# Performance work log

Measured on AMD Instinct MI355X. Metric: run time of the kernel, lower is better.

Reference implementation:

```python
import jax, jax.numpy as jnp
import numpy as np

TEMPERATURE = 0.1
NORM_EPS = 1e-12   # F.normalize default eps
LOSS_EPS = 1e-6

def _l2norm_c(x):
    # L2-normalize along channel dim (axis=1), matching F.normalize(dim=1)
    n = jnp.sqrt(jnp.sum(x * x, axis=1, keepdims=True))
    return x / jnp.maximum(n, NORM_EPS)

def setup_inputs() -> dict:
    key = jax.random.key(0)
    k1, k2, k3 = jax.random.split(key, 3)
    N, C, H, W = 8, 64, 64, 64
    rgb_map = jax.random.normal(k1, (N, C, H, W), dtype=jnp.float32)
    ir_map = jax.random.normal(k2, (N, C, H, W), dtype=jnp.float32)
    targets = jax.random.randint(k3, (N,), 0, 2)  # unused by the forward math
    return {"rgb_map": rgb_map, "ir_map": ir_map, "targets": targets}

def reference(rgb_map, ir_map, targets):
    N, C, H, W = rgb_map.shape
    rgb = _l2norm_c(rgb_map).reshape(N, C, H * W)   # [N, C, P]
    ir = _l2norm_c(ir_map).reshape(N, C, H * W)     # [N, C, P]
    # [N, P, P] similarity, then temperature exp
    logit = jnp.exp(jnp.einsum('ncp,ncq->npq', rgb, ir) / TEMPERATURE)
    pos = jnp.trace(logit, axis1=1, axis2=2)        # diagonal (positive) sum per sample
    tot = jnp.sum(logit, axis=(-1, -2))             # full row/col sum per sample
    loss = -jnp.log(pos / (tot + LOSS_EPS)).mean()
    return loss
```

## Files before the change

kernel.cpp:

```cpp
#include <hip/hip_runtime.h>

#define N_ 8
#define C_ 64
#define P_ 4096

typedef float f32x4 __attribute__((ext_vector_type(4)));
typedef float f32x2 __attribute__((ext_vector_type(2)));
typedef short bf16x8 __attribute__((ext_vector_type(8)));

__device__ __forceinline__ unsigned short f2bf(float f) {
  unsigned int u = __builtin_bit_cast(unsigned int, f);
  u = (u + 0x7fffu + ((u >> 16) & 1u)) >> 16;
  return (unsigned short)u;
}

__device__ __forceinline__ float exp2appr(float x) {
  const int i = (int)__builtin_fmaf(x, 8388608.0f, 1064992209.0f);
  return __builtin_bit_cast(float, i);
}

__global__ void __launch_bounds__(256) norm_transpose(
    const float* __restrict__ rgb, const float* __restrict__ ir,
    unsigned short* __restrict__ rgbnT, unsigned short* __restrict__ irnT) {
  const int tid = threadIdx.x;
  const int half = tid >> 7;
  const int pl = tid & 127;
  const int gp = blockIdx.x * 128 + pl;
  const int n = gp >> 12;
  const int p = gp & (P_ - 1);
  const float* src = (blockIdx.y == 0) ? rgb : ir;
  unsigned short* dst = (blockIdx.y == 0) ? rgbnT : irnT;
  const float SC = 14.4269504088896340736f;
  const float* col = src + (size_t)n * C_ * P_ + (size_t)(half * 32) * P_ + p;
  float v[32];
  float ss = 0.f;
#pragma unroll
  for (int c = 0; c < 32; ++c) {
    v[c] = col[(size_t)c * P_];
    ss += v[c] * v[c];
  }
  __shared__ float ssq[2][128];
  ssq[half][pl] = ss;
  __syncthreads();
  const float tot = ssq[0][pl] + ssq[1][pl];
  float inv = 1.0f / fmaxf(sqrtf(tot), 1e-12f);
  if (blockIdx.y == 0) inv *= SC;
  const int gx = (blockIdx.y == 0) ? 0 : (p & 7);
  unsigned short* o = dst + (size_t)gp * C_;
#pragma unroll
  for (int gi = 0; gi < 4; ++gi) {
    bf16x8 pack;
#pragma unroll
    for (int j = 0; j < 8; ++j) pack[j] = (short)f2bf(v[gi * 8 + j] * inv);
    const int gg = half * 4 + gi;
    *reinterpret_cast<bf16x8*>(o + (gg ^ gx) * 8) = pack;
  }
}

__device__ __forceinline__ void stage_tile(const unsigned short* src,
                                           unsigned short* dst, int tid,
                                           int wid) {
#pragma unroll
  for (int r = 0; r < 2; ++r) {
    __builtin_amdgcn_global_load_lds(
        (const __attribute__((address_space(1))) void*)(src +
                                                        (size_t)(r * 256 + tid) * 8),
        (__attribute__((address_space(3))) void*)(dst + (r * 256 + wid * 64) * 8),
        16, 0, 0);
  }
}

__global__ void __launch_bounds__(256) gemm_exp_reduce(
    const unsigned short* __restrict__ aT, const unsigned short* __restrict__ bT,
    float* __restrict__ partials) {
  const int lin = blockIdx.x;
  const int n = lin & 7;
  const int local = lin >> 3;
  const int pc = local & 15;
  const int qc = local >> 4;
  const int tid = threadIdx.x;
  const int lane = tid & 63;
  const int wid = tid >> 6;
  const int pbase = pc * 256 + wid * 64;
  const int q0 = qc * 512;
  const unsigned short* A = aT + (size_t)n * P_ * C_;
  const unsigned short* B = bT + (size_t)n * P_ * C_;
  const int r16 = lane & 15;
  const int kofs = (lane >> 4) * 8;

  __shared__ __align__(16) unsigned short bs0[64 * 64];
  __shared__ __align__(16) unsigned short bs1[64 * 64];
  __shared__ __align__(16) unsigned short bs2[64 * 64];
  __shared__ __align__(16) unsigned short bs3[64 * 64];

  bf16x8 af[2][4];
#pragma unroll
  for (int ks = 0; ks < 2; ++ks)
#pragma unroll
    for (int mi = 0; mi < 4; ++mi)
      af[ks][mi] = *reinterpret_cast<const bf16x8*>(
          A + (size_t)(pbase + mi * 16 + r16) * C_ + ks * 32 + kofs);

  stage_tile(B + (size_t)(q0 + 0 * 64) * C_, bs0, tid, wid);
  stage_tile(B + (size_t)(q0 + 1 * 64) * C_, bs1, tid, wid);
  stage_tile(B + (size_t)(q0 + 2 * 64) * C_, bs2, tid, wid);

  unsigned short *pcur = bs0, *pnx1 = bs1, *pnx2 = bs2, *pnx3 = bs3;

  const f32x4 zc = (f32x4)(0.f);
  f32x2 ch2[8];
#pragma unroll
  for (int k = 0; k < 8; ++k) ch2[k] = (f32x2)(0.f);
  float pos = 0.f;
  const int col = lane & 15;
  const int rowb = (lane >> 4) * 4;

#pragma unroll 1
  for (int t = 0; t < 8; ++t) {
    asm volatile("s_waitcnt vmcnt(4)" ::: "memory");
    __builtin_amdgcn_sched_barrier(0);
    __builtin_amdgcn_s_barrier();

    int s = t + 3;
    if (s >= 8) s -= 8;
    stage_tile(B + (size_t)(q0 + s * 64) * C_, pnx3, tid, wid);

    const unsigned short* bp = pcur;
    bf16x8 bf_[2][4];
#pragma unroll
    for (int ks = 0; ks < 2; ++ks)
#pragma unroll
      for (int ni = 0; ni < 4; ++ni) {
        const int row = ni * 16 + r16;
        const int seg = ks * 4 + (lane >> 4);
        bf_[ks][ni] = *reinterpret_cast<const bf16x8*>(
            bp + row * 64 + ((seg ^ (lane & 7)) * 8));
      }

    f32x4 acc[4][4];
    __builtin_amdgcn_s_setprio(1);
#pragma unroll
    for (int mi = 0; mi < 4; ++mi)
#pragma unroll
      for (int ni = 0; ni < 4; ++ni)
        acc[mi][ni] = __builtin_amdgcn_mfma_f32_16x16x32_bf16(
            af[0][mi], bf_[0][ni], zc, 0, 0, 0);
#pragma unroll
    for (int mi = 0; mi < 4; ++mi)
#pragma unroll
      for (int ni = 0; ni < 4; ++ni)
        acc[mi][ni] = __builtin_amdgcn_mfma_f32_16x16x32_bf16(
            af[1][mi], bf_[1][ni], acc[mi][ni], 0, 0, 0);
    __builtin_amdgcn_s_setprio(0);

#pragma unroll
    for (int mi = 0; mi < 4; ++mi)
#pragma unroll
      for (int ni = 0; ni < 4; ++ni) {
        const int base = ((mi * 4 + ni) & 3) * 2;
        const f32x4 v = acc[mi][ni];
        f32x2 a0, a1;
        a0[0] = v[0]; a0[1] = v[1];
        a1[0] = v[2]; a1[1] = v[3];
        const f32x2 f0 = a0 * 8388608.0f + (f32x2)(1064992209.0f);
        const f32x2 f1 = a1 * 8388608.0f + (f32x2)(1064992209.0f);
        f32x2 e0, e1;
        e0[0] = __builtin_bit_cast(float, (int)f0[0]);
        e0[1] = __builtin_bit_cast(float, (int)f0[1]);
        e1[0] = __builtin_bit_cast(float, (int)f1[0]);
        e1[1] = __builtin_bit_cast(float, (int)f1[1]);
        ch2[base] += e0;
        ch2[base + 1] += e1;
      }
    const int qb = q0 + t * 64;
    if (pbase == qb) {
#pragma unroll
      for (int mi = 0; mi < 4; ++mi)
#pragma unroll
        for (int r = 0; r < 4; ++r)
          if (rowb + r == col) pos += exp2appr(acc[mi][mi][r]);
    }

    unsigned short* tmp = pcur;
    pcur = pnx1;
    pnx1 = pnx2;
    pnx2 = pnx3;
    pnx3 = tmp;
  }

  f32x2 sum2 = ((ch2[0] + ch2[1]) + (ch2[2] + ch2[3])) +
               ((ch2[4] + ch2[5]) + (ch2[6] + ch2[7]));
  float tot = sum2[0] + sum2[1];
#pragma unroll
  for (int off = 32; off > 0; off >>= 1) {
    tot += __shfl_down(tot, off);
    pos += __shfl_down(pos, off);
  }
  __shared__ float sb[8];
  if (lane == 0) { sb[wid * 2] = pos; sb[wid * 2 + 1] = tot; }
  __syncthreads();
  if (tid == 0) {
    const float pp = sb[0] + sb[2] + sb[4] + sb[6];
    const float tt = sb[1] + sb[3] + sb[5] + sb[7];
    const int bid = n * 128 + pc * 8 + qc;
    partials[bid * 2] = pp;
    partials[bid * 2 + 1] = tt;
  }
}

__global__ void __launch_bounds__(1024) finalize(
    const float* __restrict__ partials, float* __restrict__ out) {
  const int tid = threadIdx.x;
  const int lane = tid & 63, wid = tid >> 6;
  __shared__ float sp[16], st[16], sl[8];
  const int n = tid >> 7;
  const int i = tid & 127;
  float p = partials[(n * 128 + i) * 2];
  float t = partials[(n * 128 + i) * 2 + 1];
#pragma unroll
  for (int off = 32; off > 0; off >>= 1) {
    p += __shfl_down(p, off);
    t += __shfl_down(t, off);
  }
  if (lane == 0) { sp[wid] = p; st[wid] = t; }
  __syncthreads();
  if (tid < 8) {
    const float pp = sp[2 * tid] + sp[2 * tid + 1];
    const float tt = st[2 * tid] + st[2 * tid + 1];
    sl[tid] = -logf(pp / (tt + 1e-6f));
  }
  __syncthreads();
  if (tid == 0) {
    float loss = 0.f;
#pragma unroll
    for (int k = 0; k < 8; ++k) loss += sl[k];
    out[0] = loss * (1.0f / N_);
  }
}

extern "C" void kernel_launch(void* const* d_in, const int* in_sizes, int n_in,
                              void* d_out, int out_size, void* d_ws, size_t ws_size,
                              hipStream_t stream) {
  const float* rgb = (const float*)d_in[0];
  const float* ir = (const float*)d_in[1];
  float* out = (float*)d_out;

  unsigned short* rgbnT = (unsigned short*)d_ws;
  unsigned short* irnT = rgbnT + (size_t)N_ * P_ * C_;
  float* partials = (float*)(irnT + (size_t)N_ * P_ * C_);

  dim3 g1(N_ * P_ / 128, 2);
  norm_transpose<<<g1, 256, 0, stream>>>(rgb, ir, rgbnT, irnT);

  gemm_exp_reduce<<<1024, 256, 0, stream>>>(rgbnT, irnT, partials);

  finalize<<<1, 1024, 0, stream>>>(partials, out);
}
```

Baseline: 39.28 us.

## Load B tiles straight into registers with double buffering instead of LDS staging

The GEMM kernel no longer stages B tiles into a four-deep LDS ring through global_load_lds, and drops the per-iteration block barrier. Each wave now issues its own inline-asm global_load_dwordx4 loads of its swizzled B fragments into two register buffers, prefetching the tile after next while computing the current one. The aim is to remove LDS round trips and block synchronization from the inner loop. In exchange, every wave re-reads the same B data from cache, register pressure rises, and the last iterations prefetch past the tile range instead of wrapping, which reads data that is never used.

Measured after the change: 45.42 us. +15.6%, slower.

```diff
diff --git a/kernel.cpp b/kernel.cpp
--- a/kernel.cpp
+++ b/kernel.cpp
@@ -7,6 +7,7 @@
 typedef float f32x4 __attribute__((ext_vector_type(4)));
 typedef float f32x2 __attribute__((ext_vector_type(2)));
 typedef short bf16x8 __attribute__((ext_vector_type(8)));
+typedef unsigned long long u64;
 
 __device__ __forceinline__ unsigned short f2bf(float f) {
   unsigned int u = __builtin_bit_cast(unsigned int, f);
@@ -54,19 +55,6 @@
     for (int j = 0; j < 8; ++j) pack[j] = (short)f2bf(v[gi * 8 + j] * inv);
     const int gg = half * 4 + gi;
     *reinterpret_cast<bf16x8*>(o + (gg ^ gx) * 8) = pack;
-  }
-}
-
-__device__ __forceinline__ void stage_tile(const unsigned short* src,
-                                           unsigned short* dst, int tid,
-                                           int wid) {
-#pragma unroll
-  for (int r = 0; r < 2; ++r) {
-    __builtin_amdgcn_global_load_lds(
-        (const __attribute__((address_space(1))) void*)(src +
-                                                        (size_t)(r * 256 + tid) * 8),
-        (__attribute__((address_space(3))) void*)(dst + (r * 256 + wid * 64) * 8),
-        16, 0, 0);
   }
 }
 
@@ -88,24 +76,39 @@
   const int r16 = lane & 15;
   const int kofs = (lane >> 4) * 8;
 
-  __shared__ __align__(16) unsigned short bs0[64 * 64];
-  __shared__ __align__(16) unsigned short bs1[64 * 64];
-  __shared__ __align__(16) unsigned short bs2[64 * 64];
-  __shared__ __align__(16) unsigned short bs3[64 * 64];
-
-  bf16x8 af[2][4];
+  u64 ba[8];
 #pragma unroll
   for (int ks = 0; ks < 2; ++ks)
 #pragma unroll
-    for (int mi = 0; mi < 4; ++mi)
-      af[ks][mi] = *reinterpret_cast<const bf16x8*>(
-          A + (size_t)(pbase + mi * 16 + r16) * C_ + ks * 32 + kofs);
-
-  stage_tile(B + (size_t)(q0 + 0 * 64) * C_, bs0, tid, wid);
-  stage_tile(B + (size_t)(q0 + 1 * 64) * C_, bs1, tid, wid);
-  stage_tile(B + (size_t)(q0 + 2 * 64) * C_, bs2, tid, wid);
-
-  unsigned short *pcur = bs0, *pnx1 = bs1, *pnx2 = bs2, *pnx3 = bs3;
+    for (int ni = 0; ni < 4; ++ni) {
+      const int row = ni * 16 + r16;
+      const int seg = ks * 4 + (lane >> 4);
+      const int fo = row * 128 + ((seg ^ (lane & 7)) * 16);
+      ba[ks * 4 + ni] = (u64)(size_t)B + (u64)(q0 * 128 + fo);
+    }
+
+  f32x4 af[2][4];
+#pragma unroll
+  for (int ks = 0; ks < 2; ++ks)
+#pragma unroll
+    for (int mi = 0; mi < 4; ++mi) {
+      const u64 aa = (u64)(size_t)(A + (size_t)(pbase + mi * 16 + r16) * C_ +
+                                   ks * 32 + kofs);
+      asm volatile("global_load_dwordx4 %0, %1, off"
+                   : "=v"(af[ks][mi]) : "v"(aa));
+    }
+
+  f32x4 br0[2][4], br1[2][4];
+#pragma unroll
+  for (int j = 0; j < 8; ++j)
+    asm volatile("global_load_dwordx4 %0, %1, off"
+                 : "=v"(br0[j >> 2][j & 3]) : "v"(ba[j]));
+#pragma unroll
+  for (int j = 0; j < 8; ++j)
+    asm volatile("global_load_dwordx4 %0, %1, off"
+                 : "=v"(br1[j >> 2][j & 3]) : "v"(ba[j] + 8192));
+#pragma unroll
+  for (int j = 0; j < 8; ++j) ba[j] += 16384;
 
   const f32x4 zc = (f32x4)(0.f);
   f32x2 ch2[8];
@@ -115,27 +118,12 @@
   const int col = lane & 15;
   const int rowb = (lane >> 4) * 4;
 
-#pragma unroll 1
+#pragma unroll 2
   for (int t = 0; t < 8; ++t) {
-    asm volatile("s_waitcnt vmcnt(4)" ::: "memory");
+    asm volatile("s_waitcnt vmcnt(8)" ::: "memory");
     __builtin_amdgcn_sched_barrier(0);
-    __builtin_amdgcn_s_barrier();
-
-    int s = t + 3;
-    if (s >= 8) s -= 8;
-    stage_tile(B + (size_t)(q0 + s * 64) * C_, pnx3, tid, wid);
-
-    const unsigned short* bp = pcur;
-    bf16x8 bf_[2][4];
-#pragma unroll
-    for (int ks = 0; ks < 2; ++ks)
-#pragma unroll
-      for (int ni = 0; ni < 4; ++ni) {
-        const int row = ni * 16 + r16;
-        const int seg = ks * 4 + (lane >> 4);
-        bf_[ks][ni] = *reinterpret_cast<const bf16x8*>(
-            bp + row * 64 + ((seg ^ (lane & 7)) * 8));
-      }
+
+    f32x4(&br)[2][4] = (t & 1) ? br1 : br0;
 
     f32x4 acc[4][4];
     __builtin_amdgcn_s_setprio(1);
@@ -144,13 +132,15 @@
 #pragma unroll
       for (int ni = 0; ni < 4; ++ni)
         acc[mi][ni] = __builtin_amdgcn_mfma_f32_16x16x32_bf16(
-            af[0][mi], bf_[0][ni], zc, 0, 0, 0);
+            __builtin_bit_cast(bf16x8, af[0][mi]),
+            __builtin_bit_cast(bf16x8, br[0][ni]), zc, 0, 0, 0);
 #pragma unroll
     for (int mi = 0; mi < 4; ++mi)
 #pragma unroll
       for (int ni = 0; ni < 4; ++ni)
         acc[mi][ni] = __builtin_amdgcn_mfma_f32_16x16x32_bf16(
-            af[1][mi], bf_[1][ni], acc[mi][ni], 0, 0, 0);
+            __builtin_bit_cast(bf16x8, af[1][mi]),
+            __builtin_bit_cast(bf16x8, br[1][ni]), acc[mi][ni], 0, 0, 0);
     __builtin_amdgcn_s_setprio(0);
 
 #pragma unroll
@@ -181,11 +171,13 @@
           if (rowb + r == col) pos += exp2appr(acc[mi][mi][r]);
     }
 
-    unsigned short* tmp = pcur;
-    pcur = pnx1;
-    pnx1 = pnx2;
-    pnx2 = pnx3;
-    pnx3 = tmp;
+    __builtin_amdgcn_sched_barrier(0);
+#pragma unroll
+    for (int j = 0; j < 8; ++j)
+      asm volatile("global_load_dwordx4 %0, %1, off"
+                   : "=v"(br[j >> 2][j & 3]) : "v"(ba[j]));
+#pragma unroll
+    for (int j = 0; j < 8; ++j) ba[j] += 8192;
   }
 
   f32x2 sum2 = ((ch2[0] + ch2[1]) + (ch2[2] + ch2[3])) +
```

## Fuse normalization, GEMM-exp reduction and finalize into one kernel

Applied to the files above, without the earlier changes.

Merges the three kernels into one. Each block now computes L2 norms and builds bf16 operands straight from the raw fp32 inputs: the whole 512-column B slab goes into LDS up front, and the A fragments are loaded into registers. The last block to finish, found with an atomic counter, does the final loss reduction. This removes two launches and the round-trip of the transposed bf16 intermediates through global memory. In exchange, fp32 inputs are re-read redundantly across blocks (A about 8x, B about 16x) using strided column loads. The large 64KB LDS footprint may cut occupancy, and a memset launch is added.

New measurement: 55.40 us. +41.0%, slower.

```diff
diff --git a/kernel.cpp b/kernel.cpp
--- a/kernel.cpp
+++ b/kernel.cpp
@@ -19,60 +19,10 @@
   return __builtin_bit_cast(float, i);
 }
 
-__global__ void __launch_bounds__(256) norm_transpose(
+__global__ void __launch_bounds__(256) pixcon_fused(
     const float* __restrict__ rgb, const float* __restrict__ ir,
-    unsigned short* __restrict__ rgbnT, unsigned short* __restrict__ irnT) {
-  const int tid = threadIdx.x;
-  const int half = tid >> 7;
-  const int pl = tid & 127;
-  const int gp = blockIdx.x * 128 + pl;
-  const int n = gp >> 12;
-  const int p = gp & (P_ - 1);
-  const float* src = (blockIdx.y == 0) ? rgb : ir;
-  unsigned short* dst = (blockIdx.y == 0) ? rgbnT : irnT;
-  const float SC = 14.4269504088896340736f;
-  const float* col = src + (size_t)n * C_ * P_ + (size_t)(half * 32) * P_ + p;
-  float v[32];
-  float ss = 0.f;
-#pragma unroll
-  for (int c = 0; c < 32; ++c) {
-    v[c] = col[(size_t)c * P_];
-    ss += v[c] * v[c];
-  }
-  __shared__ float ssq[2][128];
-  ssq[half][pl] = ss;
-  __syncthreads();
-  const float tot = ssq[0][pl] + ssq[1][pl];
-  float inv = 1.0f / fmaxf(sqrtf(tot), 1e-12f);
-  if (blockIdx.y == 0) inv *= SC;
-  const int gx = (blockIdx.y == 0) ? 0 : (p & 7);
-  unsigned short* o = dst + (size_t)gp * C_;
-#pragma unroll
-  for (int gi = 0; gi < 4; ++gi) {
-    bf16x8 pack;
-#pragma unroll
-    for (int j = 0; j < 8; ++j) pack[j] = (short)f2bf(v[gi * 8 + j] * inv);
-    const int gg = half * 4 + gi;
-    *reinterpret_cast<bf16x8*>(o + (gg ^ gx) * 8) = pack;
-  }
-}
-
-__device__ __forceinline__ void stage_tile(const unsigned short* src,
-                                           unsigned short* dst, int tid,
-                                           int wid) {
-#pragma unroll
-  for (int r = 0; r < 2; ++r) {
-    __builtin_amdgcn_global_load_lds(
-        (const __attribute__((address_space(1))) void*)(src +
-                                                        (size_t)(r * 256 + tid) * 8),
-        (__attribute__((address_space(3))) void*)(dst + (r * 256 + wid * 64) * 8),
-        16, 0, 0);
-  }
-}
-
-__global__ void __launch_bounds__(256) gemm_exp_reduce(
-    const unsigned short* __restrict__ aT, const unsigned short* __restrict__ bT,
-    float* __restrict__ partials) {
+    float* __restrict__ par, unsigned* __restrict__ cnt,
+    float* __restrict__ out) {
   const int lin = blockIdx.x;
   const int n = lin & 7;
   const int local = lin >> 3;
@@ -81,31 +31,83 @@
   const int tid = threadIdx.x;
   const int lane = tid & 63;
   const int wid = tid >> 6;
-  const int pbase = pc * 256 + wid * 64;
+  const int p0 = pc * 256;
   const int q0 = qc * 512;
-  const unsigned short* A = aT + (size_t)n * P_ * C_;
-  const unsigned short* B = bT + (size_t)n * P_ * C_;
+  const int pbase = p0 + wid * 64;
+  const float* Araw = rgb + (size_t)n * C_ * P_;
+  const float* Braw = ir + (size_t)n * C_ * P_;
+
+  __shared__ __align__(16) unsigned short bsm[512 * 64];
+  __shared__ float ssqA[256];
+  __shared__ float sb[8];
+  __shared__ float fp[8], ft[8];
+  __shared__ unsigned rank_s;
+
+  {
+    float ss = 0.f;
+    const float* colp = Araw + p0 + tid;
+#pragma unroll 8
+    for (int c = 0; c < 64; ++c) {
+      const float x = colp[(size_t)c * P_];
+      ss = __builtin_fmaf(x, x, ss);
+    }
+    ssqA[tid] = ss;
+  }
+
+  {
+    const float* colq = Braw + q0 + 2 * tid;
+    float ss0 = 0.f, ss1 = 0.f;
+#pragma unroll 8
+    for (int c = 0; c < 64; ++c) {
+      const f32x2 v = *reinterpret_cast<const f32x2*>(colq + (size_t)c * P_);
+      ss0 = __builtin_fmaf(v[0], v[0], ss0);
+      ss1 = __builtin_fmaf(v[1], v[1], ss1);
+    }
+    const float inv0 = 1.0f / fmaxf(sqrtf(ss0), 1e-12f);
+    const float inv1 = 1.0f / fmaxf(sqrtf(ss1), 1e-12f);
+    const int r0 = 2 * tid, r1 = 2 * tid + 1;
+    unsigned short* w0 = bsm + r0 * 64;
+    unsigned short* w1 = bsm + r1 * 64;
+#pragma unroll 1
+    for (int g = 0; g < 8; ++g) {
+      bf16x8 pk0, pk1;
+#pragma unroll
+      for (int j = 0; j < 8; ++j) {
+        const f32x2 v =
+            *reinterpret_cast<const f32x2*>(colq + (size_t)(g * 8 + j) * P_);
+        pk0[j] = (short)f2bf(v[0] * inv0);
+        pk1[j] = (short)f2bf(v[1] * inv1);
+      }
+      *reinterpret_cast<bf16x8*>(w0 + ((g ^ (r0 & 7)) * 8)) = pk0;
+      *reinterpret_cast<bf16x8*>(w1 + ((g ^ (r1 & 7)) * 8)) = pk1;
+    }
+  }
+
+  __syncthreads();
+
   const int r16 = lane & 15;
   const int kofs = (lane >> 4) * 8;
-
-  __shared__ __align__(16) unsigned short bs0[64 * 64];
-  __shared__ __align__(16) unsigned short bs1[64 * 64];
-  __shared__ __align__(16) unsigned short bs2[64 * 64];
-  __shared__ __align__(16) unsigned short bs3[64 * 64];
-
+  const float SC = 14.4269504088896340736f;
+  float invA[4];
+#pragma unroll
+  for (int mi = 0; mi < 4; ++mi) {
+    const int rrel = wid * 64 + mi * 16 + r16;
+    invA[mi] = SC / fmaxf(sqrtf(ssqA[rrel]), 1e-12f);
+  }
   bf16x8 af[2][4];
 #pragma unroll
   for (int ks = 0; ks < 2; ++ks)
 #pragma unroll
-    for (int mi = 0; mi < 4; ++mi)
-      af[ks][mi] = *reinterpret_cast<const bf16x8*>(
-          A + (size_t)(pbase + mi * 16 + r16) * C_ + ks * 32 + kofs);
-
-  stage_tile(B + (size_t)(q0 + 0 * 64) * C_, bs0, tid, wid);
-  stage_tile(B + (size_t)(q0 + 1 * 64) * C_, bs1, tid, wid);
-  stage_tile(B + (size_t)(q0 + 2 * 64) * C_, bs2, tid, wid);
-
-  unsigned short *pcur = bs0, *pnx1 = bs1, *pnx2 = bs2, *pnx3 = bs3;
+    for (int mi = 0; mi < 4; ++mi) {
+      const float* src = Araw + pbase + mi * 16 + r16;
+      bf16x8 pk;
+#pragma unroll
+      for (int j = 0; j < 8; ++j) {
+        const float x = src[(size_t)(ks * 32 + kofs + j) * P_];
+        pk[j] = (short)f2bf(x * invA[mi]);
+      }
+      af[ks][mi] = pk;
+    }
 
   const f32x4 zc = (f32x4)(0.f);
   f32x2 ch2[8];
@@ -117,15 +119,7 @@
 
 #pragma unroll 1
   for (int t = 0; t < 8; ++t) {
-    asm volatile("s_waitcnt vmcnt(4)" ::: "memory");
-    __builtin_amdgcn_sched_barrier(0);
-    __builtin_amdgcn_s_barrier();
-
-    int s = t + 3;
-    if (s >= 8) s -= 8;
-    stage_tile(B + (size_t)(q0 + s * 64) * C_, pnx3, tid, wid);
-
-    const unsigned short* bp = pcur;
+    const unsigned short* bp = bsm + t * 64 * 64;
     bf16x8 bf_[2][4];
 #pragma unroll
     for (int ks = 0; ks < 2; ++ks)
@@ -180,12 +174,6 @@
         for (int r = 0; r < 4; ++r)
           if (rowb + r == col) pos += exp2appr(acc[mi][mi][r]);
     }
-
-    unsigned short* tmp = pcur;
-    pcur = pnx1;
-    pnx1 = pnx2;
-    pnx2 = pnx3;
-    pnx3 = tmp;
   }
 
   f32x2 sum2 = ((ch2[0] + ch2[1]) + (ch2[2] + ch2[3])) +
@@ -196,45 +184,41 @@
     tot += __shfl_down(tot, off);
     pos += __shfl_down(pos, off);
   }
-  __shared__ float sb[8];
   if (lane == 0) { sb[wid * 2] = pos; sb[wid * 2 + 1] = tot; }
   __syncthreads();
+
   if (tid == 0) {
     const float pp = sb[0] + sb[2] + sb[4] + sb[6];
     const float tt = sb[1] + sb[3] + sb[5] + sb[7];
-    const int bid = n * 128 + pc * 8 + qc;
-    partials[bid * 2] = pp;
-    partials[bid * 2 + 1] = tt;
-  }
-}
-
-__global__ void __launch_bounds__(1024) finalize(
-    const float* __restrict__ partials, float* __restrict__ out) {
-  const int tid = threadIdx.x;
-  const int lane = tid & 63, wid = tid >> 6;
-  __shared__ float sp[16], st[16], sl[8];
-  const int n = tid >> 7;
-  const int i = tid & 127;
-  float p = partials[(n * 128 + i) * 2];
-  float t = partials[(n * 128 + i) * 2 + 1];
-#pragma unroll
-  for (int off = 32; off > 0; off >>= 1) {
-    p += __shfl_down(p, off);
-    t += __shfl_down(t, off);
-  }
-  if (lane == 0) { sp[wid] = p; st[wid] = t; }
+    const int slot = n * 128 + pc * 8 + qc;
+    atomicAdd(&par[slot], pp);
+    atomicAdd(&par[1024 + slot], tt);
+    asm volatile("s_waitcnt vmcnt(0)" ::: "memory");
+    rank_s = atomicAdd(cnt, 1u);
+  }
   __syncthreads();
-  if (tid < 8) {
-    const float pp = sp[2 * tid] + sp[2 * tid + 1];
-    const float tt = st[2 * tid] + st[2 * tid + 1];
-    sl[tid] = -logf(pp / (tt + 1e-6f));
-  }
-  __syncthreads();
-  if (tid == 0) {
-    float loss = 0.f;
-#pragma unroll
-    for (int k = 0; k < 8; ++k) loss += sl[k];
-    out[0] = loss * (1.0f / N_);
+  if (rank_s == 1023u) {
+    const int nn = tid >> 5;
+    const int ch = tid & 31;
+    float sp_ = 0.f, st_ = 0.f;
+#pragma unroll
+    for (int k = 0; k < 4; ++k) {
+      sp_ += atomicAdd(&par[nn * 128 + ch * 4 + k], 0.0f);
+      st_ += atomicAdd(&par[1024 + nn * 128 + ch * 4 + k], 0.0f);
+    }
+#pragma unroll
+    for (int off = 16; off > 0; off >>= 1) {
+      sp_ += __shfl_down(sp_, off);
+      st_ += __shfl_down(st_, off);
+    }
+    if (ch == 0) { fp[nn] = sp_; ft[nn] = st_; }
+    __syncthreads();
+    if (tid == 0) {
+      float loss = 0.f;
+#pragma unroll
+      for (int k = 0; k < 8; ++k) loss += -logf(fp[k] / (ft[k] + 1e-6f));
+      out[0] = loss * 0.125f;
+    }
   }
 }
 
@@ -245,14 +229,10 @@
   const float* ir = (const float*)d_in[1];
   float* out = (float*)d_out;
 
-  unsigned short* rgbnT = (unsigned short*)d_ws;
-  unsigned short* irnT = rgbnT + (size_t)N_ * P_ * C_;
-  float* partials = (float*)(irnT + (size_t)N_ * P_ * C_);
-
-  dim3 g1(N_ * P_ / 128, 2);
-  norm_transpose<<<g1, 256, 0, stream>>>(rgb, ir, rgbnT, irnT);
-
-  gemm_exp_reduce<<<1024, 256, 0, stream>>>(rgbnT, irnT, partials);
-
-  finalize<<<1, 1024, 0, stream>>>(partials, out);
-}
+  float* par = (float*)d_ws;
+  unsigned* cnt = (unsigned*)(par + 2048);
+
+  hipMemsetAsync(d_ws, 0, 2048 * sizeof(float) + sizeof(unsigned), stream);
+
+  pixcon_fused<<<1024, 256, 0, stream>>>(rgb, ir, par, cnt, out);
+}
```

## Fuse finalize into GEMM via last-block atomic reduction and preload full B tile

Applied to the files above, without the earlier changes.

Removes the separate finalize kernel: each GEMM block atomically writes its partial sums and bumps a counter, and the last block to finish reduces all partials and writes the loss. The four-buffer software pipeline for B is also replaced by loading the whole 512x64 B slab into LDS up front (64 KB) and then running the loop with no per-iteration waits or barriers. This saves a kernel launch and the pipeline synchronisation, but adds a memset launch and atomics. The larger LDS footprint may lower occupancy, and nothing overlaps the up-front load.

New measurement: 46.39 us. +18.1%, slower.

```diff
diff --git a/kernel.cpp b/kernel.cpp
--- a/kernel.cpp
+++ b/kernel.cpp
@@ -57,22 +57,10 @@
   }
 }
 
-__device__ __forceinline__ void stage_tile(const unsigned short* src,
-                                           unsigned short* dst, int tid,
-                                           int wid) {
-#pragma unroll
-  for (int r = 0; r < 2; ++r) {
-    __builtin_amdgcn_global_load_lds(
-        (const __attribute__((address_space(1))) void*)(src +
-                                                        (size_t)(r * 256 + tid) * 8),
-        (__attribute__((address_space(3))) void*)(dst + (r * 256 + wid * 64) * 8),
-        16, 0, 0);
-  }
-}
-
-__global__ void __launch_bounds__(256) gemm_exp_reduce(
+__global__ void __launch_bounds__(256) gemm_fused(
     const unsigned short* __restrict__ aT, const unsigned short* __restrict__ bT,
-    float* __restrict__ partials) {
+    float* __restrict__ par, unsigned* __restrict__ cnt,
+    float* __restrict__ out) {
   const int lin = blockIdx.x;
   const int n = lin & 7;
   const int local = lin >> 3;
@@ -88,10 +76,23 @@
   const int r16 = lane & 15;
   const int kofs = (lane >> 4) * 8;
 
-  __shared__ __align__(16) unsigned short bs0[64 * 64];
-  __shared__ __align__(16) unsigned short bs1[64 * 64];
-  __shared__ __align__(16) unsigned short bs2[64 * 64];
-  __shared__ __align__(16) unsigned short bs3[64 * 64];
+  __shared__ __align__(16) unsigned short bsm[512 * 64];
+  __shared__ float sb[8];
+  __shared__ float fp[8], ft[8];
+  __shared__ unsigned rank_s;
+
+  {
+    const unsigned short* src = B + (size_t)q0 * C_;
+#pragma unroll
+    for (int r = 0; r < 16; ++r) {
+      __builtin_amdgcn_global_load_lds(
+          (const __attribute__((address_space(1))) void*)(src +
+                                                          (size_t)(r * 256 + tid) * 8),
+          (__attribute__((address_space(3))) void*)(bsm +
+                                                    (r * 256 + wid * 64) * 8),
+          16, 0, 0);
+    }
+  }
 
   bf16x8 af[2][4];
 #pragma unroll
@@ -101,11 +102,8 @@
       af[ks][mi] = *reinterpret_cast<const bf16x8*>(
           A + (size_t)(pbase + mi * 16 + r16) * C_ + ks * 32 + kofs);
 
-  stage_tile(B + (size_t)(q0 + 0 * 64) * C_, bs0, tid, wid);
-  stage_tile(B + (size_t)(q0 + 1 * 64) * C_, bs1, tid, wid);
-  stage_tile(B + (size_t)(q0 + 2 * 64) * C_, bs2, tid, wid);
-
-  unsigned short *pcur = bs0, *pnx1 = bs1, *pnx2 = bs2, *pnx3 = bs3;
+  asm volatile("s_waitcnt vmcnt(0)" ::: "memory");
+  __builtin_amdgcn_s_barrier();
 
   const f32x4 zc = (f32x4)(0.f);
   f32x2 ch2[8];
@@ -117,15 +115,7 @@
 
 #pragma unroll 1
   for (int t = 0; t < 8; ++t) {
-    asm volatile("s_waitcnt vmcnt(4)" ::: "memory");
-    __builtin_amdgcn_sched_barrier(0);
-    __builtin_amdgcn_s_barrier();
-
-    int s = t + 3;
-    if (s >= 8) s -= 8;
-    stage_tile(B + (size_t)(q0 + s * 64) * C_, pnx3, tid, wid);
-
-    const unsigned short* bp = pcur;
+    const unsigned short* bp = bsm + t * 64 * 64;
     bf16x8 bf_[2][4];
 #pragma unroll
     for (int ks = 0; ks < 2; ++ks)
@@ -180,12 +170,6 @@
         for (int r = 0; r < 4; ++r)
           if (rowb + r == col) pos += exp2appr(acc[mi][mi][r]);
     }
-
-    unsigned short* tmp = pcur;
-    pcur = pnx1;
-    pnx1 = pnx2;
-    pnx2 = pnx3;
-    pnx3 = tmp;
   }
 
   f32x2 sum2 = ((ch2[0] + ch2[1]) + (ch2[2] + ch2[3])) +
@@ -196,45 +180,41 @@
     tot += __shfl_down(tot, off);
     pos += __shfl_down(pos, off);
   }
-  __shared__ float sb[8];
   if (lane == 0) { sb[wid * 2] = pos; sb[wid * 2 + 1] = tot; }
   __syncthreads();
+
   if (tid == 0) {
     const float pp = sb[0] + sb[2] + sb[4] + sb[6];
     const float tt = sb[1] + sb[3] + sb[5] + sb[7];
-    const int bid = n * 128 + pc * 8 + qc;
-    partials[bid * 2] = pp;
-    partials[bid * 2 + 1] = tt;
-  }
-}
-
-__global__ void __launch_bounds__(1024) finalize(
-    const float* __restrict__ partials, float* __restrict__ out) {
-  const int tid = threadIdx.x;
-  const int lane = tid & 63, wid = tid >> 6;
-  __shared__ float sp[16], st[16], sl[8];
-  const int n = tid >> 7;
-  const int i = tid & 127;
-  float p = partials[(n * 128 + i) * 2];
-  float t = partials[(n * 128 + i) * 2 + 1];
-#pragma unroll
-  for (int off = 32; off > 0; off >>= 1) {
-    p += __shfl_down(p, off);
-    t += __shfl_down(t, off);
-  }
-  if (lane == 0) { sp[wid] = p; st[wid] = t; }
+    const int slot = n * 128 + pc * 8 + qc;
+    atomicAdd(&par[slot], pp);
+    atomicAdd(&par[1024 + slot], tt);
+    asm volatile("s_waitcnt vmcnt(0)" ::: "memory");
+    rank_s = atomicAdd(cnt, 1u);
+  }
   __syncthreads();
-  if (tid < 8) {
-    const float pp = sp[2 * tid] + sp[2 * tid + 1];
-    const float tt = st[2 * tid] + st[2 * tid + 1];
-    sl[tid] = -logf(pp / (tt + 1e-6f));
-  }
-  __syncthreads();
-  if (tid == 0) {
-    float loss = 0.f;
-#pragma unroll
-    for (int k = 0; k < 8; ++k) loss += sl[k];
-    out[0] = loss * (1.0f / N_);
+  if (rank_s == 1023u) {
+    const int nn = tid >> 5;
+    const int ch = tid & 31;
+    float sp_ = 0.f, st_ = 0.f;
+#pragma unroll
+    for (int k = 0; k < 4; ++k) {
+      sp_ += atomicAdd(&par[nn * 128 + ch * 4 + k], 0.0f);
+      st_ += atomicAdd(&par[1024 + nn * 128 + ch * 4 + k], 0.0f);
+    }
+#pragma unroll
+    for (int off = 16; off > 0; off >>= 1) {
+      sp_ += __shfl_down(sp_, off);
+      st_ += __shfl_down(st_, off);
+    }
+    if (ch == 0) { fp[nn] = sp_; ft[nn] = st_; }
+    __syncthreads();
+    if (tid == 0) {
+      float loss = 0.f;
+#pragma unroll
+      for (int k = 0; k < 8; ++k) loss += -logf(fp[k] / (ft[k] + 1e-6f));
+      out[0] = loss * 0.125f;
+    }
   }
 }
 
@@ -247,12 +227,13 @@
 
   unsigned short* rgbnT = (unsigned short*)d_ws;
   unsigned short* irnT = rgbnT + (size_t)N_ * P_ * C_;
-  float* partials = (float*)(irnT + (size_t)N_ * P_ * C_);
+  float* par = (float*)(irnT + (size_t)N_ * P_ * C_);
+  unsigned* cnt = (unsigned*)(par + 2048);
+
+  hipMemsetAsync(par, 0, 2048 * sizeof(float) + sizeof(unsigned), stream);
 
   dim3 g1(N_ * P_ / 128, 2);
   norm_transpose<<<g1, 256, 0, stream>>>(rgb, ir, rgbnT, irnT);
 
-  gemm_exp_reduce<<<1024, 256, 0, stream>>>(rgbnT, irnT, partials);
-
-  finalize<<<1, 1024, 0, stream>>>(partials, out);
-}
+  gemm_fused<<<1024, 256, 0, stream>>>(rgbnT, irnT, par, cnt, out);
+}
```
